# Performance work log

Hardware: AMD Instinct MI355X
Metric: run time of the kernel (lower is better)

Reference implementation:

```python
import jax, jax.numpy as jnp
import numpy as np

N = 25000      # nodes
E = 400000     # edges
IN = 1024      # in_channels
FC = 128       # feature_channels
ADD = 20       # additional_channels
MID = (FC + ADD) // 4   # 37, fc1 output (heads=4)
OUT = 3
EPS = 1e-5
NEG_SLOPE = 0.01


def setup_inputs() -> dict:
    key = jax.random.key(0)
    ks = jax.random.split(key, 16)
    d = {}
    d["features"] = jax.random.normal(ks[0], (N, IN), dtype=jnp.float32)
    d["edges"] = jax.random.randint(ks[1], (2, E), 0, N, dtype=jnp.int64)
    d["edges2"] = jax.random.randint(ks[2], (2, 1000), 0, N, dtype=jnp.int64)
    d["edge_features"] = jax.random.normal(ks[3], (E, 1), dtype=jnp.float32)
    d["additional_feature"] = jax.random.normal(ks[4], (N, ADD), dtype=jnp.float32)
    # SAGEConv params: lin_l (neighbor path, with bias), lin_r (root path, no bias)
    s = 1.0 / np.sqrt(IN)
    d["Wl"] = jax.random.uniform(ks[5], (FC, IN), jnp.float32, -s, s)
    d["bl"] = jax.random.uniform(ks[6], (FC,), jnp.float32, -s, s)
    d["Wr"] = jax.random.uniform(ks[7], (FC, IN), jnp.float32, -s, s)
    s1 = 1.0 / np.sqrt(FC + ADD)
    d["W1"] = jax.random.uniform(ks[8], (MID, FC + ADD), jnp.float32, -s1, s1)
    d["b1"] = jax.random.uniform(ks[9], (MID,), jnp.float32, -s1, s1)
    s2 = 1.0 / np.sqrt(MID)
    d["W2"] = jax.random.uniform(ks[10], (OUT, MID), jnp.float32, -s2, s2)
    d["b2"] = jax.random.uniform(ks[11], (OUT,), jnp.float32, -s2, s2)
    # BatchNorm1d (eval mode -> running stats)
    d["gamma"] = jnp.ones((MID,), jnp.float32)
    d["beta"] = jnp.zeros((MID,), jnp.float32)
    d["run_mean"] = jax.random.normal(ks[12], (MID,), dtype=jnp.float32) * 0.1
    d["run_var"] = jnp.abs(jax.random.normal(ks[13], (MID,), dtype=jnp.float32)) * 0.1 + 1.0
    return d


def reference(features, edges, edges2, edge_features, additional_feature,
              Wl, bl, Wr, W1, b1, W2, b2, gamma, beta, run_mean, run_var):
    src, dst = edges[0], edges[1]  # PyG: messages flow source -> target
    # scatter-mean of neighbor features onto targets
    agg = jax.ops.segment_sum(features[src], dst, num_segments=N)        # [N, IN]
    deg = jax.ops.segment_sum(jnp.ones((E,), features.dtype), dst, num_segments=N)
    agg = agg / jnp.maximum(deg, 1.0)[:, None]
    # SAGEConv: lin_l(mean_neigh) + lin_r(x)
    x = agg @ Wl.T + bl + features @ Wr.T                                 # [N, FC]
    x = jnp.where(x >= 0, x, NEG_SLOPE * x)                               # leaky_relu
    # dropout is identity in eval mode
    x = jnp.concatenate([x, additional_feature], axis=1) @ W1.T + b1      # [N, MID]
    x = jnp.maximum(x, 0.0)                                               # relu
    x = gamma * (x - run_mean) * jax.lax.rsqrt(run_var + EPS) + beta      # BN eval
    return x @ W2.T + b2                                                  # [N, OUT]
```

## Files before the change

### kernel.cpp

```cpp
#include <hip/hip_runtime.h>

#define N_NODES 25000
#define N_EDGES 400000
#define IN_CH 1024
#define FC 128
#define ADD_CH 20
#define XCH 148
#define MID 37
#define OUT_CH 3
#define MAXDEG 64
#define CSTRIDE 16

typedef short bf16x8 __attribute__((ext_vector_type(8)));
typedef float f32x4 __attribute__((ext_vector_type(4)));

__device__ __forceinline__ float bflo(unsigned int v) {
    return __builtin_bit_cast(float, v << 16);
}
__device__ __forceinline__ float bfhi(unsigned int v) {
    return __builtin_bit_cast(float, v & 0xffff0000u);
}
__device__ __forceinline__ unsigned int cvtpk(float a, float b) {
    unsigned int r;
    asm("v_cvt_pk_bf16_f32 %0, %1, %2" : "=v"(r) : "v"(a), "v"(b));
    return r;
}

__device__ __forceinline__ void gload16(const void* g, void* l) {
    __builtin_amdgcn_global_load_lds(
        (const __attribute__((address_space(1))) unsigned int*)g,
        (__attribute__((address_space(3))) unsigned int*)l,
        16, 0, 0);
}

#define WSWZ_B 16
#define ZERO_B 49

__global__ __launch_bounds__(512) void prep(const float* __restrict__ Wl,
                                            const float* __restrict__ Wr,
                                            ushort* __restrict__ Wpk,
                                            int* __restrict__ cursor) {
    int b = blockIdx.x, t = threadIdx.x;
    if (b < WSWZ_B) {
        int w = t >> 6, lane = t & 63, l15 = lane & 15, q8 = (lane >> 4) * 8;
        int ch = b * 16 + l15;
        const float* src = (ch < FC) ? (Wl + (size_t)ch * IN_CH)
                                     : (Wr + (size_t)(ch - FC) * IN_CH);
        #pragma unroll
        for (int j = 0; j < 4; ++j) {
            int kt = w * 4 + j;
            float4 lo = *(const float4*)(src + kt * 32 + q8);
            float4 hi = *(const float4*)(src + kt * 32 + q8 + 4);
            uint4 pk;
            pk.x = cvtpk(lo.x, lo.y); pk.y = cvtpk(lo.z, lo.w);
            pk.z = cvtpk(hi.x, hi.y); pk.w = cvtpk(hi.z, hi.w);
            ((uint4*)Wpk)[((size_t)kt * 16 + b) * 64 + lane] = pk;
        }
    } else {
        int i = (b - WSWZ_B) * 512 + t;
        if (i < N_NODES) {
            uint4 z = {0, 0, 0, 0};
            uint4* dst = (uint4*)(cursor + (size_t)i * CSTRIDE);
            dst[0] = z; dst[1] = z; dst[2] = z; dst[3] = z;
        }
    }
}

#define GEMM_B 391
#define BUILD_B 782

__global__ __launch_bounds__(512, 4) void gemm_build(const float* __restrict__ A,
                                                     const ushort* __restrict__ Wpk,
                                                     ushort* __restrict__ Py,
                                                     ushort* __restrict__ Pz,
                                                     const int* __restrict__ edges,
                                                     int* __restrict__ cursor,
                                                     int* __restrict__ col) {
    __shared__ uint4 LDS[2][1536];
    int b = blockIdx.x, t = threadIdx.x;
    if (b >= GEMM_B) {
        int e = (b - GEMM_B) * 512 + t;
        if (e < N_EDGES) {
            int dst = edges[N_EDGES + e];
            int pos = atomicAdd(&cursor[(size_t)dst * CSTRIDE], 1);
            if (pos < MAXDEG) col[dst * MAXDEG + pos] = edges[e];
        }
        return;
    }
    int m0 = b * 64;

    int ga = t >> 7, hq = (t >> 6) & 1, la = t & 63;
    int nodeA = m0 + ga * 16 + (la & 15);
    if (nodeA >= N_NODES) nodeA = N_NODES - 1;
    const float* Asrc = A + (size_t)nodeA * IN_CH + (la >> 4) * 8 + hq * 4;
    const uint4* Wg = (const uint4*)Wpk;
    int tb = t & ~63;

    int w = t >> 6, lane = t & 63;
    int wm = w >> 2, wn = w & 3;
    int l15 = lane & 15, q = lane >> 4;

    f32x4 acc[4][2] = {};

    gload16(Wg + t,       &LDS[0][tb]);
    gload16(Wg + 512 + t, &LDS[0][512 + tb]);
    gload16(Asrc,         &LDS[0][1024 + tb]);
    __syncthreads();

    #define COMPUTE(cur)                                                          \
    {                                                                             \
        bf16x8 wf[4];                                                             \
        _Pragma("unroll")                                                         \
        for (int i = 0; i < 4; ++i)                                               \
            wf[i] = *(const bf16x8*)&LDS[cur][(wn * 4 + i) * 64 + lane];          \
        bf16x8 af[2];                                                             \
        _Pragma("unroll")                                                         \
        for (int g2 = 0; g2 < 2; ++g2) {                                          \
            f32x4 lo = *(const f32x4*)&LDS[cur][1024 + ((wm * 2 + g2) * 2 + 0) * 64 + lane]; \
            f32x4 hi = *(const f32x4*)&LDS[cur][1024 + ((wm * 2 + g2) * 2 + 1) * 64 + lane]; \
            uint4 pk;                                                             \
            pk.x = cvtpk(lo[0], lo[1]); pk.y = cvtpk(lo[2], lo[3]);               \
            pk.z = cvtpk(hi[0], hi[1]); pk.w = cvtpk(hi[2], hi[3]);               \
            af[g2] = __builtin_bit_cast(bf16x8, pk);                              \
        }                                                                         \
        _Pragma("unroll")                                                         \
        for (int i = 0; i < 4; ++i)                                               \
            _Pragma("unroll")                                                     \
            for (int g2 = 0; g2 < 2; ++g2)                                        \
                acc[i][g2] = __builtin_amdgcn_mfma_f32_16x16x32_bf16(wf[i], af[g2], acc[i][g2], 0, 0, 0); \
    }

    for (int c = 0; c < 31; ++c) {
        int cur = c & 1;
        const uint4* ws = Wg + (size_t)(c + 1) * 1024;
        gload16(ws + t,       &LDS[cur ^ 1][tb]);
        gload16(ws + 512 + t, &LDS[cur ^ 1][512 + tb]);
        gload16(Asrc + (size_t)(c + 1) * 32, &LDS[cur ^ 1][1024 + tb]);
        asm volatile("s_waitcnt vmcnt(3)" ::: "memory");
        __builtin_amdgcn_sched_barrier(0);
        __builtin_amdgcn_s_barrier();
        __builtin_amdgcn_sched_barrier(0);
        COMPUTE(cur);
        __builtin_amdgcn_s_barrier();
        __builtin_amdgcn_sched_barrier(0);
    }
    asm volatile("s_waitcnt vmcnt(0)" ::: "memory");
    __builtin_amdgcn_sched_barrier(0);
    __builtin_amdgcn_s_barrier();
    __builtin_amdgcn_sched_barrier(0);
    COMPUTE(1);
    #undef COMPUTE

    #pragma unroll
    for (int g2 = 0; g2 < 2; ++g2) {
        int node = m0 + wm * 32 + g2 * 16 + l15;
        if (node < N_NODES) {
            ushort* base = (wn < 2) ? (Py + (size_t)node * FC + (wn & 1) * 64 + q * 4)
                                    : (Pz + (size_t)node * FC + (wn & 1) * 64 + q * 4);
            #pragma unroll
            for (int i = 0; i < 4; ++i) {
                f32x4 v = acc[i][g2];
                uint2 pk;
                pk.x = cvtpk(v[0], v[1]);
                pk.y = cvtpk(v[2], v[3]);
                *(uint2*)(base + i * 16) = pk;
            }
        }
    }
}

__global__ __launch_bounds__(512) void fused_tail(const ushort* __restrict__ Py,
                                                  const ushort* __restrict__ Pz,
                                                  const int* __restrict__ deg,
                                                  const int* __restrict__ col,
                                                  const float* __restrict__ addf,
                                                  const float* __restrict__ bl,
                                                  const float* __restrict__ W1,
                                                  const float* __restrict__ b1,
                                                  const float* __restrict__ W2,
                                                  const float* __restrict__ b2,
                                                  const float* __restrict__ gamma,
                                                  const float* __restrict__ beta,
                                                  const float* __restrict__ rmean,
                                                  const float* __restrict__ rvar,
                                                  float* __restrict__ out) {
    __shared__ float W1s[XCH][MID + 3];
    __shared__ float xbuf[8][XCH + 4];
    __shared__ float hbuf[8][MID + 3];
    int t = threadIdx.x;
    for (int idx = t; idx < MID * XCH; idx += 512) {
        int j = idx / XCH, k = idx - j * XCH;
        W1s[k][j] = W1[idx];
    }
    __syncthreads();
    int w = t >> 6, lane = t & 63;
    int n = blockIdx.x * 8 + w;
    bool valid = (n < N_NODES);
    int d = valid ? deg[(size_t)n * CSTRIDE] : 0;
    if (d > MAXDEG) d = MAXDEG;
    int g = lane >> 4, c16 = lane & 15;
    float s[8] = {0.f, 0.f, 0.f, 0.f, 0.f, 0.f, 0.f, 0.f};
    if (d > 0) {
        int cidx = col[n * MAXDEG + (lane < d ? lane : 0)];
        for (int i = 0; i < d; i += 16) {
            int e[4];
            uint4 v[4];
            #pragma unroll
            for (int j = 0; j < 4; ++j) {
                int ee = i + g + j * 4;
                e[j] = __shfl(cidx, (ee < d) ? ee : 0);
            }
            #pragma unroll
            for (int j = 0; j < 4; ++j)
                v[j] = *(const uint4*)&Py[(size_t)e[j] * FC + c16 * 8];
            #pragma unroll
            for (int j = 0; j < 4; ++j) {
                if (i + g + j * 4 < d) {
                    s[0] += bflo(v[j].x); s[1] += bfhi(v[j].x);
                    s[2] += bflo(v[j].y); s[3] += bfhi(v[j].y);
                    s[4] += bflo(v[j].z); s[5] += bfhi(v[j].z);
                    s[6] += bflo(v[j].w); s[7] += bfhi(v[j].w);
                }
            }
        }
        #pragma unroll
        for (int r = 0; r < 8; ++r) {
            s[r] += __shfl_xor(s[r], 16);
            s[r] += __shfl_xor(s[r], 32);
        }
    }
    if (valid) {
        if (lane < 16) {
            #pragma unroll
            for (int r = 0; r < 8; ++r) xbuf[w][lane * 8 + r] = s[r];
        }
        float invd = 1.0f / (float)(d > 1 ? d : 1);
        unsigned int vr = *(const unsigned int*)&Pz[(size_t)n * FC + lane * 2];
        float x0 = xbuf[w][2 * lane] * invd + bl[2 * lane] + bflo(vr);
        float x1 = xbuf[w][2 * lane + 1] * invd + bl[2 * lane + 1] + bfhi(vr);
        x0 = (x0 >= 0.f) ? x0 : 0.01f * x0;
        x1 = (x1 >= 0.f) ? x1 : 0.01f * x1;
        xbuf[w][2 * lane] = x0;
        xbuf[w][2 * lane + 1] = x1;
        if (lane < ADD_CH) xbuf[w][FC + lane] = addf[(size_t)n * ADD_CH + lane];
        if (lane < MID) {
            float h = b1[lane];
            #pragma unroll 4
            for (int k = 0; k < XCH; ++k) h += W1s[k][lane] * xbuf[w][k];
            h = fmaxf(h, 0.0f);
            h = gamma[lane] * (h - rmean[lane]) * rsqrtf(rvar[lane] + 1e-5f) + beta[lane];
            hbuf[w][lane] = h;
        }
        if (lane < OUT_CH) {
            float o = b2[lane];
            #pragma unroll
            for (int j = 0; j < MID; ++j) o += W2[lane * MID + j] * hbuf[w][j];
            out[(size_t)n * OUT_CH + lane] = o;
        }
    }
}


extern "C" void kernel_launch(void* const* d_in, const int* in_sizes, int n_in,
                              void* d_out, int out_size, void* d_ws, size_t ws_size,
                              hipStream_t stream) {
    const float* features = (const float*)d_in[0];
    const int*   edges    = (const int*)d_in[1];
    const float* addf     = (const float*)d_in[4];
    const float* Wl       = (const float*)d_in[5];
    const float* bl       = (const float*)d_in[6];
    const float* Wr       = (const float*)d_in[7];
    const float* W1       = (const float*)d_in[8];
    const float* b1       = (const float*)d_in[9];
    const float* W2       = (const float*)d_in[10];
    const float* b2       = (const float*)d_in[11];
    const float* gamma    = (const float*)d_in[12];
    const float* beta     = (const float*)d_in[13];
    const float* rmean    = (const float*)d_in[14];
    const float* rvar     = (const float*)d_in[15];
    float* out = (float*)d_out;

    char* ws = (char*)d_ws;
    size_t off = 0;
    ushort* Py = (ushort*)(ws + off);     off += (size_t)N_NODES * FC * 2;
    ushort* Pz = (ushort*)(ws + off);     off += (size_t)N_NODES * FC * 2;
    ushort* Wpk = (ushort*)(ws + off);    off += (size_t)32 * 16 * 64 * 16;
    int* cursor = (int*)(ws + off);       off += (size_t)N_NODES * CSTRIDE * 4;
    int* col = (int*)(ws + off);          off += (size_t)N_NODES * MAXDEG * 4;

    prep<<<WSWZ_B + ZERO_B, 512, 0, stream>>>(Wl, Wr, Wpk, cursor);

    gemm_build<<<GEMM_B + BUILD_B, 512, 0, stream>>>(features, Wpk, Py, Pz,
                                                     edges, cursor, col);

    fused_tail<<<(N_NODES + 7) / 8, 512, 0, stream>>>(Py, Pz, cursor, col, addf, bl,
                                                      W1, b1, W2, b2, gamma, beta,
                                                      rmean, rvar, out);
}
```

Measured before the change: 265.4 us.

## Triple-buffer GEMM LDS pipeline and batch four edges per build thread

The GEMM main loop moves from double to triple buffering in LDS. Loads run two chunks ahead, with vmcnt waits adjusted, so more global-load latency is hidden behind MFMA work. The edge-bucketing blocks now handle four edges per thread, issuing all loads and then all atomics so memory operations overlap, which cuts the build block count. LDS per block grows to 72KB, which may lower occupancy below the four blocks per CU targeted by the launch bounds.

```diff
diff --git a/kernel.cpp b/kernel.cpp
--- a/kernel.cpp
+++ b/kernel.cpp
@@ -67,7 +67,7 @@
 }
 
 #define GEMM_B 391
-#define BUILD_B 782
+#define BUILD_B 196
 
 __global__ __launch_bounds__(512, 4) void gemm_build(const float* __restrict__ A,
                                                      const ushort* __restrict__ Wpk,
@@ -76,14 +76,29 @@
                                                      const int* __restrict__ edges,
                                                      int* __restrict__ cursor,
                                                      int* __restrict__ col) {
-    __shared__ uint4 LDS[2][1536];
+    __shared__ uint4 LDS[3][1536];
     int b = blockIdx.x, t = threadIdx.x;
     if (b >= GEMM_B) {
-        int e = (b - GEMM_B) * 512 + t;
-        if (e < N_EDGES) {
-            int dst = edges[N_EDGES + e];
-            int pos = atomicAdd(&cursor[(size_t)dst * CSTRIDE], 1);
-            if (pos < MAXDEG) col[dst * MAXDEG + pos] = edges[e];
+        int base = (b - GEMM_B) * 2048 + t;
+        int src[4], dst[4], pos[4];
+        #pragma unroll
+        for (int k = 0; k < 4; ++k) {
+            int e = base + k * 512;
+            bool v = (e < N_EDGES);
+            dst[k] = v ? edges[N_EDGES + e] : 0;
+            src[k] = v ? edges[e] : 0;
+        }
+        #pragma unroll
+        for (int k = 0; k < 4; ++k) {
+            int e = base + k * 512;
+            if (e < N_EDGES)
+                pos[k] = atomicAdd(&cursor[(size_t)dst[k] * CSTRIDE], 1);
+        }
+        #pragma unroll
+        for (int k = 0; k < 4; ++k) {
+            int e = base + k * 512;
+            if (e < N_EDGES && pos[k] < MAXDEG)
+                col[dst[k] * MAXDEG + pos[k]] = src[k];
         }
         return;
     }
@@ -102,22 +117,24 @@
 
     f32x4 acc[4][2] = {};
 
-    gload16(Wg + t,       &LDS[0][tb]);
-    gload16(Wg + 512 + t, &LDS[0][512 + tb]);
-    gload16(Asrc,         &LDS[0][1024 + tb]);
-    __syncthreads();
-
-    #define COMPUTE(cur)                                                          \
+    gload16(Wg + t,        &LDS[0][tb]);
+    gload16(Wg + 512 + t,  &LDS[0][512 + tb]);
+    gload16(Asrc,          &LDS[0][1024 + tb]);
+    gload16(Wg + 1024 + t,       &LDS[1][tb]);
+    gload16(Wg + 1024 + 512 + t, &LDS[1][512 + tb]);
+    gload16(Asrc + 32,           &LDS[1][1024 + tb]);
+
+    #define COMPUTE(bc)                                                           \
     {                                                                             \
         bf16x8 wf[4];                                                             \
         _Pragma("unroll")                                                         \
         for (int i = 0; i < 4; ++i)                                               \
-            wf[i] = *(const bf16x8*)&LDS[cur][(wn * 4 + i) * 64 + lane];          \
+            wf[i] = *(const bf16x8*)&LDS[bc][(wn * 4 + i) * 64 + lane];           \
         bf16x8 af[2];                                                             \
         _Pragma("unroll")                                                         \
         for (int g2 = 0; g2 < 2; ++g2) {                                          \
-            f32x4 lo = *(const f32x4*)&LDS[cur][1024 + ((wm * 2 + g2) * 2 + 0) * 64 + lane]; \
-            f32x4 hi = *(const f32x4*)&LDS[cur][1024 + ((wm * 2 + g2) * 2 + 1) * 64 + lane]; \
+            f32x4 lo = *(const f32x4*)&LDS[bc][1024 + ((wm * 2 + g2) * 2 + 0) * 64 + lane]; \
+            f32x4 hi = *(const f32x4*)&LDS[bc][1024 + ((wm * 2 + g2) * 2 + 1) * 64 + lane]; \
             uint4 pk;                                                             \
             pk.x = cvtpk(lo[0], lo[1]); pk.y = cvtpk(lo[2], lo[3]);               \
             pk.z = cvtpk(hi[0], hi[1]); pk.w = cvtpk(hi[2], hi[3]);               \
@@ -130,25 +147,33 @@
                 acc[i][g2] = __builtin_amdgcn_mfma_f32_16x16x32_bf16(wf[i], af[g2], acc[i][g2], 0, 0, 0); \
     }
 
-    for (int c = 0; c < 31; ++c) {
-        int cur = c & 1;
-        const uint4* ws = Wg + (size_t)(c + 1) * 1024;
-        gload16(ws + t,       &LDS[cur ^ 1][tb]);
-        gload16(ws + 512 + t, &LDS[cur ^ 1][512 + tb]);
-        gload16(Asrc + (size_t)(c + 1) * 32, &LDS[cur ^ 1][1024 + tb]);
-        asm volatile("s_waitcnt vmcnt(3)" ::: "memory");
+    int bc = 0, bs = 2;
+    for (int c = 0; c < 30; ++c) {
+        const uint4* ws = Wg + (size_t)(c + 2) * 1024;
+        gload16(ws + t,       &LDS[bs][tb]);
+        gload16(ws + 512 + t, &LDS[bs][512 + tb]);
+        gload16(Asrc + (size_t)(c + 2) * 32, &LDS[bs][1024 + tb]);
+        asm volatile("s_waitcnt vmcnt(6)" ::: "memory");
         __builtin_amdgcn_sched_barrier(0);
         __builtin_amdgcn_s_barrier();
         __builtin_amdgcn_sched_barrier(0);
-        COMPUTE(cur);
+        COMPUTE(bc);
         __builtin_amdgcn_s_barrier();
         __builtin_amdgcn_sched_barrier(0);
-    }
+        bc = (bc == 2) ? 0 : bc + 1;
+        bs = (bs == 2) ? 0 : bs + 1;
+    }
+    asm volatile("s_waitcnt vmcnt(3)" ::: "memory");
+    __builtin_amdgcn_sched_barrier(0);
+    __builtin_amdgcn_s_barrier();
+    __builtin_amdgcn_sched_barrier(0);
+    COMPUTE(bc);
+    bc = (bc == 2) ? 0 : bc + 1;
     asm volatile("s_waitcnt vmcnt(0)" ::: "memory");
     __builtin_amdgcn_sched_barrier(0);
     __builtin_amdgcn_s_barrier();
     __builtin_amdgcn_sched_barrier(0);
-    COMPUTE(1);
+    COMPUTE(bc);
     #undef COMPUTE
 
     #pragma unroll
```

Measured after the change: 255.0 us. -3.9%, faster.
